# Kernel tuning notes

Measured on AMD Instinct MI355X. Metric: run time of the kernel, lower is better.

The kernel has to match this reference:

```python
import jax, jax.numpy as jnp
import numpy as np

B, S, A, MSG, C = 524288, 64, 16, 32, 4
CH = 9 + S  # children_states feature dim = 73
EPS = 1e-12  # F.normalize clamp_min eps


def _l2norm(v):
    n = jnp.sqrt(jnp.sum(v * v, axis=-1, keepdims=True))
    return v / jnp.maximum(n, EPS)


def setup_inputs() -> dict:
    key = jax.random.key(0)
    ks = jax.random.split(key, 12)
    def lin(kw, kb, out_d, in_d):
        bound = 1.0 / np.sqrt(in_d)
        W = jax.random.uniform(kw, (out_d, in_d), minval=-bound, maxval=bound, dtype=jnp.float32)
        b = jax.random.uniform(kb, (out_d,), minval=-bound, maxval=bound, dtype=jnp.float32)
        return W, b
    W1, b1 = lin(ks[0], ks[1], 64, S + A)
    W2, b2 = lin(ks[2], ks[3], 64, 64 + MSG)
    W3, b3 = lin(ks[4], ks[5], MSG, 64)
    Wa, ba = lin(ks[6], ks[7], MSG, CH)
    return {
        "x": jax.random.normal(ks[8], (B, S), dtype=jnp.float32),
        "u": jax.random.normal(ks[9], (B, A), dtype=jnp.float32),
        "children_states": jax.random.normal(ks[10], (B, C, CH), dtype=jnp.float32),
        "m": jax.random.normal(ks[11], (B, C * MSG), dtype=jnp.float32),
        "W1": W1, "b1": b1, "W2": W2, "b2": b2, "W3": W3, "b3": b3,
        "Wa": Wa, "ba": ba,
    }


def reference(x, u, children_states, m, W1, b1, W2, b2, W3, b3, Wa, ba):
    # fc1 on cat(x, u), then L2 normalize
    xu = jnp.concatenate([x, u], axis=-1) @ W1.T + b1          # [B, 64]
    xu = _l2norm(xu)
    # attention over children (softmax along child axis, dim=-2)
    att = jax.nn.softmax(children_states @ Wa.T + ba, axis=-2)  # [B, C, MSG]
    mm = m.reshape(*children_states.shape[:-1], -1)             # [B, C, MSG]
    magg = jnp.sum(mm * att, axis=-2)                           # [B, MSG]
    # fused MLP tail
    xum = jnp.tanh(jnp.concatenate([xu, magg], axis=-1))        # [B, 64+MSG]
    xum = jnp.tanh(xum @ W2.T + b2)                             # [B, 64]
    xum = xum @ W3.T + b3                                       # [B, MSG]
    return _l2norm(xum)
```

## Files before the change

### kernel.cpp

```cpp
#include <hip/hip_runtime.h>
#include <cstddef>

typedef __fp16 f16x8 __attribute__((ext_vector_type(8)));
typedef float f32x4 __attribute__((ext_vector_type(4)));
typedef unsigned int uint32;
typedef unsigned short ushort;

constexpr int S = 64, MSG = 32, CH = 73;

constexpr int FC1_OFF = 0;
constexpr int ATT_OFF = 12 * 512;
constexpr int FC2_OFF = 18 * 512;
constexpr int FC3_OFF = 30 * 512;
constexpr int WS_ELEMS = 34 * 512;

__global__ void prep_pack(const float* __restrict__ W1, const float* __restrict__ b1,
                          const float* __restrict__ Wa, const float* __restrict__ ba,
                          const float* __restrict__ W2, const float* __restrict__ W3,
                          ushort* __restrict__ wsf) {
  int idx = blockIdx.x * 256 + threadIdx.x;
  if (idx >= WS_ELEMS) return;
  int tile = idx >> 9;
  int lane = (idx >> 3) & 63;
  int e = idx & 7;
  int jloc = lane & 15;
  int kloc = ((lane >> 4) << 3) + e;
  float v = 0.f;
  if (tile < 12) {
    int t = tile >> 2, f = tile & 3;
    int j = f * 16 + jloc, k = t * 32 + kloc;
    v = (k < 80) ? W1[j * 80 + k] : (k == 80 ? b1[j] : 0.f);
  } else if (tile < 18) {
    int q = tile - 12, t = q >> 1, f = q & 1;
    int j = f * 16 + jloc, k = t * 32 + kloc;
    v = (k < 73) ? Wa[j * 73 + k] : (k == 73 ? ba[j] : 0.f);
  } else if (tile < 30) {
    int q = tile - 18, t = q >> 2, f = q & 3;
    int j = f * 16 + jloc, k = t * 32 + kloc;
    v = W2[j * 96 + k];
  } else {
    int q = tile - 30, t = q >> 1, f = q & 1;
    int j = f * 16 + jloc, k = t * 32 + kloc;
    v = W3[j * 64 + k];
  }
  union { __fp16 h; ushort s; } cv;
  cv.h = (__fp16)v;
  wsf[idx] = cv.s;
}

__device__ __forceinline__ f32x4 mf(f16x8 a, f16x8 b, f32x4 c) {
  return __builtin_amdgcn_mfma_f32_16x16x32_f16(a, b, c, 0, 0, 0);
}
__device__ __forceinline__ uint32 pku(float a, float b) {
  auto r = __builtin_amdgcn_cvt_pkrtz(a, b);
  union { decltype(r) f; uint32 u; } v; v.f = r; return v.u;
}
__device__ __forceinline__ f16x8 packA(const float* f) {
  union { uint32 u[4]; f16x8 h; } r;
  r.u[0] = pku(f[0], f[1]); r.u[1] = pku(f[2], f[3]);
  r.u[2] = pku(f[4], f[5]); r.u[3] = pku(f[6], f[7]);
  return r.h;
}
__device__ __forceinline__ float fast_tanh(float v) {
  v = fminf(15.f, fmaxf(-15.f, v));
  float t = __expf(2.f * v);
  return (t - 1.f) * __builtin_amdgcn_rcpf(t + 1.f);
}

__launch_bounds__(256)
__global__ void critic_mfma_kernel(
    const float* __restrict__ x, const float* __restrict__ u,
    const float* __restrict__ cs, const float* __restrict__ m,
    const float* __restrict__ b2, const float* __restrict__ b3,
    const ushort* __restrict__ wsf, float* __restrict__ out, int n) {
  __shared__ __attribute__((aligned(16))) __fp16 hbuf[4][16 * 96];
  __shared__ __attribute__((aligned(16))) __fp16 h2buf[4][16 * 64];

  const int wave = threadIdx.x >> 6;
  const int lane = threadIdx.x & 63;
  const int lm = lane & 15;
  const int lq = lane >> 4;
  const int r0 = (blockIdx.x * 4 + wave) * 16;
  if (r0 >= n) return;

  __fp16* __restrict__ ht = &hbuf[wave][0];
  __fp16* __restrict__ h2t = &h2buf[wave][0];

  auto ldB = [&](int off_tile) -> f16x8 {
    return *reinterpret_cast<const f16x8*>(wsf + off_tile + lane * 8);
  };

  f16x8 wa[6];
#pragma unroll
  for (int i = 0; i < 6; ++i) wa[i] = ldB(ATT_OFF + i * 512);

#pragma unroll
  for (int g = 0; g < 4; ++g) {
    const int bb = r0 + 4 * g + (lm >> 2);
    const int cc = lm & 3;
    const float* __restrict__ csrow = cs + ((size_t)bb * 4 + cc) * CH;
    f32x4 zac[2] = {{0.f, 0.f, 0.f, 0.f}, {0.f, 0.f, 0.f, 0.f}};
#pragma unroll
    for (int t = 0; t < 3; ++t) {
      float f[8];
      const int kbase = t * 32 + lq * 8;
#pragma unroll
      for (int e = 0; e < 8; ++e) {
        int k = kbase + e;
        f[e] = (t < 2) ? csrow[k]
                       : ((k < 73) ? csrow[k] : (k == 73 ? 1.f : 0.f));
      }
      f16x8 af = packA(f);
      zac[0] = mf(af, wa[t * 2 + 0], zac[0]);
      zac[1] = mf(af, wa[t * 2 + 1], zac[1]);
    }
    const int bo = r0 + 4 * g + lq;
    const float* __restrict__ mrow = m + (size_t)bo * 128;
#pragma unroll
    for (int f = 0; f < 2; ++f) {
      const int j = lm + 16 * f;
      float e0 = __expf(zac[f][0]);
      float e1 = __expf(zac[f][1]);
      float e2 = __expf(zac[f][2]);
      float e3 = __expf(zac[f][3]);
      float den = (e0 + e1) + (e2 + e3);
      float num = fmaf(mrow[0 * 32 + j], e0,
                  fmaf(mrow[1 * 32 + j], e1,
                  fmaf(mrow[2 * 32 + j], e2, mrow[3 * 32 + j] * e3)));
      float mg = num * __builtin_amdgcn_rcpf(den);
      ht[(4 * g + lq) * 96 + 64 + j] = (__fp16)fast_tanh(mg);
    }
  }

  f32x4 hac[4] = {{0.f,0.f,0.f,0.f},{0.f,0.f,0.f,0.f},{0.f,0.f,0.f,0.f},{0.f,0.f,0.f,0.f}};
  {
    const float* __restrict__ xrow = x + (size_t)(r0 + lm) * S;
    const float* __restrict__ urow = u + (size_t)(r0 + lm) * 16;
#pragma unroll
    for (int t = 0; t < 2; ++t) {
      const float4* p = reinterpret_cast<const float4*>(xrow + t * 32 + lq * 8);
      float4 va = p[0], vb = p[1];
      float f[8] = {va.x, va.y, va.z, va.w, vb.x, vb.y, vb.z, vb.w};
      f16x8 af = packA(f);
#pragma unroll
      for (int fi = 0; fi < 4; ++fi)
        hac[fi] = mf(af, ldB(FC1_OFF + (t * 4 + fi) * 512), hac[fi]);
    }
    {
      float f[8];
      const int kbase = 64 + lq * 8;
#pragma unroll
      for (int e = 0; e < 8; ++e) {
        int k = kbase + e;
        f[e] = (k < 80) ? urow[k - 64] : (k == 80 ? 1.f : 0.f);
      }
      f16x8 af = packA(f);
#pragma unroll
      for (int fi = 0; fi < 4; ++fi)
        hac[fi] = mf(af, ldB(FC1_OFF + (2 * 4 + fi) * 512), hac[fi]);
    }
  }
  {
    float rn[4];
#pragma unroll
    for (int reg = 0; reg < 4; ++reg) {
      float s = hac[0][reg] * hac[0][reg];
      s = fmaf(hac[1][reg], hac[1][reg], s);
      s = fmaf(hac[2][reg], hac[2][reg], s);
      s = fmaf(hac[3][reg], hac[3][reg], s);
      s += __shfl_xor(s, 1);
      s += __shfl_xor(s, 2);
      s += __shfl_xor(s, 4);
      s += __shfl_xor(s, 8);
      rn[reg] = __builtin_amdgcn_rcpf(fmaxf(sqrtf(s), 1e-12f));
    }
#pragma unroll
    for (int fi = 0; fi < 4; ++fi)
#pragma unroll
      for (int reg = 0; reg < 4; ++reg)
        ht[(4 * lq + reg) * 96 + lm + 16 * fi] =
            (__fp16)fast_tanh(hac[fi][reg] * rn[reg]);
  }

  {
    f32x4 ac2[4] = {{0.f,0.f,0.f,0.f},{0.f,0.f,0.f,0.f},{0.f,0.f,0.f,0.f},{0.f,0.f,0.f,0.f}};
    f16x8 a2[3];
#pragma unroll
    for (int t = 0; t < 3; ++t)
      a2[t] = *reinterpret_cast<const f16x8*>(ht + lm * 96 + t * 32 + lq * 8);
#pragma unroll
    for (int t = 0; t < 3; ++t)
#pragma unroll
      for (int fi = 0; fi < 4; ++fi)
        ac2[fi] = mf(a2[t], ldB(FC2_OFF + (t * 4 + fi) * 512), ac2[fi]);
#pragma unroll
    for (int fi = 0; fi < 4; ++fi) {
      float bv = b2[lm + 16 * fi];
#pragma unroll
      for (int reg = 0; reg < 4; ++reg)
        h2t[(4 * lq + reg) * 64 + lm + 16 * fi] =
            (__fp16)fast_tanh(ac2[fi][reg] + bv);
    }
  }

  {
    f32x4 o[2] = {{0.f,0.f,0.f,0.f},{0.f,0.f,0.f,0.f}};
    f16x8 a3[2];
#pragma unroll
    for (int t = 0; t < 2; ++t)
      a3[t] = *reinterpret_cast<const f16x8*>(h2t + lm * 64 + t * 32 + lq * 8);
#pragma unroll
    for (int t = 0; t < 2; ++t)
#pragma unroll
      for (int fi = 0; fi < 2; ++fi)
        o[fi] = mf(a3[t], ldB(FC3_OFF + (t * 2 + fi) * 512), o[fi]);
#pragma unroll
    for (int fi = 0; fi < 2; ++fi) {
      float bv = b3[lm + 16 * fi];
#pragma unroll
      for (int reg = 0; reg < 4; ++reg) o[fi][reg] += bv;
    }
    float rn2[4];
#pragma unroll
    for (int reg = 0; reg < 4; ++reg) {
      float s = fmaf(o[0][reg], o[0][reg], o[1][reg] * o[1][reg]);
      s += __shfl_xor(s, 1);
      s += __shfl_xor(s, 2);
      s += __shfl_xor(s, 4);
      s += __shfl_xor(s, 8);
      rn2[reg] = __builtin_amdgcn_rcpf(fmaxf(sqrtf(s), 1e-12f));
    }
#pragma unroll
    for (int fi = 0; fi < 2; ++fi)
#pragma unroll
      for (int reg = 0; reg < 4; ++reg)
        out[(size_t)(r0 + 4 * lq + reg) * MSG + lm + 16 * fi] =
            o[fi][reg] * rn2[reg];
  }
}

extern "C" void kernel_launch(void* const* d_in, const int* in_sizes, int n_in,
                              void* d_out, int out_size, void* d_ws, size_t ws_size,
                              hipStream_t stream) {
  const float* x  = (const float*)d_in[0];
  const float* u  = (const float*)d_in[1];
  const float* cs = (const float*)d_in[2];
  const float* m  = (const float*)d_in[3];
  const float* W1 = (const float*)d_in[4];
  const float* b1 = (const float*)d_in[5];
  const float* W2 = (const float*)d_in[6];
  const float* b2 = (const float*)d_in[7];
  const float* W3 = (const float*)d_in[8];
  const float* b3 = (const float*)d_in[9];
  const float* Wa = (const float*)d_in[10];
  const float* ba = (const float*)d_in[11];
  float* out = (float*)d_out;
  ushort* wsf = (ushort*)d_ws;

  const int n = in_sizes[0] / S;

  hipLaunchKernelGGL(prep_pack, dim3((WS_ELEMS + 255) / 256), dim3(256), 0, stream,
                     W1, b1, Wa, ba, W2, W3, wsf);

  const int blocks = (n + 63) / 64;
  hipLaunchKernelGGL(critic_mfma_kernel, dim3(blocks), dim3(256), 0, stream,
                     x, u, cs, m, b2, b3, wsf, out, n);
}
```

Measured before the change: 271.5 us.

## Stage children_states via coalesced LDS copy, prefetch x/u, pad LDS strides

Each wave now copies its 16-row block of children_states (16×73 floats) into LDS with coalesced float4 loads, instead of each lane doing strided scalar global loads. The x and u rows are loaded as float4 at kernel start so their latency overlaps the attention phase. The hbuf and h2buf row strides are padded (96→104, 64→72) to reduce LDS bank conflicts on the f16x8 reads. In exchange the kernel uses more LDS, which may lower occupancy, and it relies on 16-byte alignment of the block offset (16*73*4 bytes, which is aligned).

```diff
diff --git a/kernel.cpp b/kernel.cpp
--- a/kernel.cpp
+++ b/kernel.cpp
@@ -61,11 +61,20 @@
   r.u[2] = pku(f[4], f[5]); r.u[3] = pku(f[6], f[7]);
   return r.h;
 }
+__device__ __forceinline__ f16x8 packA2(float4 a, float4 b) {
+  union { uint32 u[4]; f16x8 h; } r;
+  r.u[0] = pku(a.x, a.y); r.u[1] = pku(a.z, a.w);
+  r.u[2] = pku(b.x, b.y); r.u[3] = pku(b.z, b.w);
+  return r.h;
+}
 __device__ __forceinline__ float fast_tanh(float v) {
   v = fminf(15.f, fmaxf(-15.f, v));
   float t = __expf(2.f * v);
   return (t - 1.f) * __builtin_amdgcn_rcpf(t + 1.f);
 }
+
+constexpr int HT_LD = 104;
+constexpr int H2_LD = 72;
 
 __launch_bounds__(256)
 __global__ void critic_mfma_kernel(
@@ -73,8 +82,9 @@
     const float* __restrict__ cs, const float* __restrict__ m,
     const float* __restrict__ b2, const float* __restrict__ b3,
     const ushort* __restrict__ wsf, float* __restrict__ out, int n) {
-  __shared__ __attribute__((aligned(16))) __fp16 hbuf[4][16 * 96];
-  __shared__ __attribute__((aligned(16))) __fp16 h2buf[4][16 * 64];
+  __shared__ __attribute__((aligned(16))) float csb[4][1168];
+  __shared__ __attribute__((aligned(16))) __fp16 hbuf[4][16 * HT_LD];
+  __shared__ __attribute__((aligned(16))) __fp16 h2buf[4][16 * H2_LD];
 
   const int wave = threadIdx.x >> 6;
   const int lane = threadIdx.x & 63;
@@ -83,8 +93,18 @@
   const int r0 = (blockIdx.x * 4 + wave) * 16;
   if (r0 >= n) return;
 
+  float* __restrict__ csw = &csb[wave][0];
   __fp16* __restrict__ ht = &hbuf[wave][0];
   __fp16* __restrict__ h2t = &h2buf[wave][0];
+
+  const float4* __restrict__ xrow4 =
+      reinterpret_cast<const float4*>(x + (size_t)(r0 + lm) * S);
+  float4 xva = xrow4[2 * lq], xvb = xrow4[2 * lq + 1];
+  float4 xvc = xrow4[8 + 2 * lq], xvd = xrow4[9 + 2 * lq];
+  const int uq = (lq < 2) ? lq : 0;
+  const float4* __restrict__ urow4 =
+      reinterpret_cast<const float4*>(u + (size_t)(r0 + lm) * 16);
+  float4 uva = urow4[2 * uq], uvb = urow4[2 * uq + 1];
 
   auto ldB = [&](int off_tile) -> f16x8 {
     return *reinterpret_cast<const f16x8*>(wsf + off_tile + lane * 8);
@@ -96,9 +116,15 @@
 
 #pragma unroll
   for (int g = 0; g < 4; ++g) {
-    const int bb = r0 + 4 * g + (lm >> 2);
-    const int cc = lm & 3;
-    const float* __restrict__ csrow = cs + ((size_t)bb * 4 + cc) * CH;
+    {
+      const float4* __restrict__ src =
+          reinterpret_cast<const float4*>(cs + (size_t)(r0 * 4 + 16 * g) * CH);
+      float4* __restrict__ dst = reinterpret_cast<float4*>(csw);
+#pragma unroll
+      for (int i = 0; i < 4; ++i) dst[i * 64 + lane] = src[i * 64 + lane];
+      if (lane < 36) dst[256 + lane] = src[256 + lane];
+    }
+    const float* __restrict__ crow = csw + lm * CH;
     f32x4 zac[2] = {{0.f, 0.f, 0.f, 0.f}, {0.f, 0.f, 0.f, 0.f}};
 #pragma unroll
     for (int t = 0; t < 3; ++t) {
@@ -107,8 +133,7 @@
 #pragma unroll
       for (int e = 0; e < 8; ++e) {
         int k = kbase + e;
-        f[e] = (t < 2) ? csrow[k]
-                       : ((k < 73) ? csrow[k] : (k == 73 ? 1.f : 0.f));
+        f[e] = (k < 73) ? crow[k] : (k == 73 ? 1.f : 0.f);
       }
       f16x8 af = packA(f);
       zac[0] = mf(af, wa[t * 2 + 0], zac[0]);
@@ -128,37 +153,28 @@
                   fmaf(mrow[1 * 32 + j], e1,
                   fmaf(mrow[2 * 32 + j], e2, mrow[3 * 32 + j] * e3)));
       float mg = num * __builtin_amdgcn_rcpf(den);
-      ht[(4 * g + lq) * 96 + 64 + j] = (__fp16)fast_tanh(mg);
+      ht[(4 * g + lq) * HT_LD + 64 + j] = (__fp16)fast_tanh(mg);
     }
   }
 
   f32x4 hac[4] = {{0.f,0.f,0.f,0.f},{0.f,0.f,0.f,0.f},{0.f,0.f,0.f,0.f},{0.f,0.f,0.f,0.f}};
   {
-    const float* __restrict__ xrow = x + (size_t)(r0 + lm) * S;
-    const float* __restrict__ urow = u + (size_t)(r0 + lm) * 16;
-#pragma unroll
-    for (int t = 0; t < 2; ++t) {
-      const float4* p = reinterpret_cast<const float4*>(xrow + t * 32 + lq * 8);
-      float4 va = p[0], vb = p[1];
-      float f[8] = {va.x, va.y, va.z, va.w, vb.x, vb.y, vb.z, vb.w};
-      f16x8 af = packA(f);
-#pragma unroll
-      for (int fi = 0; fi < 4; ++fi)
-        hac[fi] = mf(af, ldB(FC1_OFF + (t * 4 + fi) * 512), hac[fi]);
-    }
-    {
-      float f[8];
-      const int kbase = 64 + lq * 8;
-#pragma unroll
-      for (int e = 0; e < 8; ++e) {
-        int k = kbase + e;
-        f[e] = (k < 80) ? urow[k - 64] : (k == 80 ? 1.f : 0.f);
-      }
-      f16x8 af = packA(f);
-#pragma unroll
-      for (int fi = 0; fi < 4; ++fi)
-        hac[fi] = mf(af, ldB(FC1_OFF + (2 * 4 + fi) * 512), hac[fi]);
-    }
+    f16x8 a0 = packA2(xva, xvb);
+    f16x8 a1 = packA2(xvc, xvd);
+#pragma unroll
+    for (int fi = 0; fi < 4; ++fi) hac[fi] = mf(a0, ldB(FC1_OFF + fi * 512), hac[fi]);
+#pragma unroll
+    for (int fi = 0; fi < 4; ++fi) hac[fi] = mf(a1, ldB(FC1_OFF + (4 + fi) * 512), hac[fi]);
+    float f[8];
+    float uf[8] = {uva.x, uva.y, uva.z, uva.w, uvb.x, uvb.y, uvb.z, uvb.w};
+#pragma unroll
+    for (int e = 0; e < 8; ++e) {
+      int k = 64 + lq * 8 + e;
+      f[e] = (k < 80) ? ((lq < 2) ? uf[e] : 0.f) : (k == 80 ? 1.f : 0.f);
+    }
+    f16x8 a2f = packA(f);
+#pragma unroll
+    for (int fi = 0; fi < 4; ++fi) hac[fi] = mf(a2f, ldB(FC1_OFF + (8 + fi) * 512), hac[fi]);
   }
   {
     float rn[4];
@@ -178,7 +194,7 @@
     for (int fi = 0; fi < 4; ++fi)
 #pragma unroll
       for (int reg = 0; reg < 4; ++reg)
-        ht[(4 * lq + reg) * 96 + lm + 16 * fi] =
+        ht[(4 * lq + reg) * HT_LD + lm + 16 * fi] =
             (__fp16)fast_tanh(hac[fi][reg] * rn[reg]);
   }
 
@@ -187,7 +203,7 @@
     f16x8 a2[3];
 #pragma unroll
     for (int t = 0; t < 3; ++t)
-      a2[t] = *reinterpret_cast<const f16x8*>(ht + lm * 96 + t * 32 + lq * 8);
+      a2[t] = *reinterpret_cast<const f16x8*>(ht + lm * HT_LD + t * 32 + lq * 8);
 #pragma unroll
     for (int t = 0; t < 3; ++t)
 #pragma unroll
@@ -198,7 +214,7 @@
       float bv = b2[lm + 16 * fi];
 #pragma unroll
       for (int reg = 0; reg < 4; ++reg)
-        h2t[(4 * lq + reg) * 64 + lm + 16 * fi] =
+        h2t[(4 * lq + reg) * H2_LD + lm + 16 * fi] =
             (__fp16)fast_tanh(ac2[fi][reg] + bv);
     }
   }
@@ -208,7 +224,7 @@
     f16x8 a3[2];
 #pragma unroll
     for (int t = 0; t < 2; ++t)
-      a3[t] = *reinterpret_cast<const f16x8*>(h2t + lm * 64 + t * 32 + lq * 8);
+      a3[t] = *reinterpret_cast<const f16x8*>(h2t + lm * H2_LD + t * 32 + lq * 8);
 #pragma unroll
     for (int t = 0; t < 2; ++t)
 #pragma unroll
```

New measurement: 231.7 us. -14.7%, faster.
